# Kernel tuning notes

Hardware: AMD Instinct MI355X
Metric: run time of the kernel (lower is better)

Reference implementation:

```python
import jax, jax.numpy as jnp
import numpy as np

DIM = 256; CTX_DIM = 256; K = 7; SK = 5; NH = 4  # num_heads*2
HD = DIM // NH; SCALE = HD ** -0.5
H = 64; W = 64; HC = 56; WC = 56
LN_EPS = 1e-6; BN_EPS = 1e-5


def make_bias_idx(k, h, w):
    # Faithful port of ContMix.generate_idx + apply_rpb index construction.
    rs = 2 * k - 1
    idx_h = np.arange(k); idx_w = np.arange(k)
    idx_k = (idx_h[:, None] * rs + idx_w).reshape(-1)
    rep_h = np.ones(k, np.int64); rep_h[k // 2] = h - (k - 1)
    rep_w = np.ones(k, np.int64); rep_w[k // 2] = w - (k - 1)
    bias_hw = np.repeat(idx_h, rep_h)[:, None] * rs + np.repeat(idx_w, rep_w)  # (h, w)
    bias_idx = (bias_hw[..., None] + idx_k).reshape(-1, k * k)                 # (h*w, k^2)
    return jnp.asarray(bias_idx[::-1].copy())  # torch.flip along dim 0


def window_idx(n, k):
    # NATTEN-style clamped neighborhood window starts.
    s = np.clip(np.arange(n) - k // 2, 0, n - k)
    return jnp.asarray(s[:, None] + np.arange(k))  # (n, k)


BIDX1 = make_bias_idx(SK, H, W)
BIDX2 = make_bias_idx(K, H, W)
IDXI_S = window_idx(H, SK); IDXJ_S = window_idx(W, SK)
IDXI_L = window_idx(H, K);  IDXJ_L = window_idx(W, K)


def ln2d(x, g, b):
    # LayerNorm over channel dim per spatial location, x: (B, C, H, W)
    mu = x.mean(1, keepdims=True)
    var = ((x - mu) ** 2).mean(1, keepdims=True)
    return (x - mu) * jax.lax.rsqrt(var + LN_EPS) * g[None, :, None, None] + b[None, :, None, None]


def conv1x1(x, Wt):
    return jnp.einsum('oc,bchw->bohw', Wt, x)


def apply_rpb(attn, rpb, bias_idx, h, w):
    g = rpb.shape[0]
    r = rpb.reshape(g, -1)[:, bias_idx]  # (g, h*w, k^2)
    return attn + r.reshape(1, g, h, w, -1)


def na2d_av(attn, value, k, idx_i, idx_j):
    # attn: (B, G, H, W, k^2), value: (B, G, H, W, C)
    B, G, h, w, _ = attn.shape
    v = value[:, :, idx_i]        # (B, G, H, k, W, C)
    v = v[:, :, :, :, idx_j]      # (B, G, H, k, W, k, C)
    a = attn.reshape(B, G, h, w, k, k)
    return jnp.einsum('bghwpq,bghpwqc->bghwc', a, v)


def contmix_forward(x, ctx, Wq, gq, bq, Wk, gk, bk, Wproj, rpb1, rpb2, Wdy, bn_g, bn_b):
    B = x.shape[0]
    q = ln2d(conv1x1(x, Wq), gq, bq) * SCALE                       # (B, DIM, H, W)
    # AdaptiveAvgPool2d(7) on 56x56 -> exact 8x8 bins
    kctx = ctx.reshape(B, CTX_DIM, 7, HC // 7, 7, WC // 7).mean((3, 5))
    kf = ln2d(conv1x1(kctx, Wk), gk, bk)                            # (B, DIM, 7, 7)
    q = q.reshape(B, NH, HD, H * W)
    kf = kf.reshape(B, NH, HD, 49)
    wgt = jnp.einsum('bgcn,bgcl->bgnl', q, kf)                      # (B, 4, HW, 49)
    wgt = jnp.einsum('ml,bgnl->bgnm', Wproj, wgt)                   # (B, 4, HW, 74)
    wgt = wgt.reshape(B, NH, H, W, SK * SK + K * K)
    attn1 = wgt[:, :NH // 2, :, :, :SK * SK]                        # group1, 25
    attn2 = wgt[:, NH // 2:, :, :, SK * SK:]                        # group2, 49
    attn1 = jax.nn.softmax(apply_rpb(attn1, rpb1, BIDX1, H, W), -1)
    attn2 = jax.nn.softmax(apply_rpb(attn2, rpb2, BIDX2, H, W), -1)
    # 'b (m g c) h w -> m b g h w c', m=2, g=2
    v = x.reshape(B, 2, NH // 2, HD, H, W).transpose(1, 0, 2, 4, 5, 3)
    x1 = na2d_av(attn1, v[0], SK, IDXI_S, IDXJ_S)                   # (B, 2, H, W, HD)
    x2 = na2d_av(attn2, v[1], K, IDXI_L, IDXJ_L)
    out = jnp.concatenate([x1, x2], axis=1)                         # (B, 4, H, W, HD)
    out = out.transpose(0, 1, 4, 2, 3).reshape(B, DIM, H, W)
    out = conv1x1(out, Wdy)
    # BatchNorm2d in eval mode: running_mean=0, running_var=1
    out = out * (bn_g * jax.lax.rsqrt(jnp.float32(1.0) + BN_EPS))[None, :, None, None] + bn_b[None, :, None, None]
    return out


def setup_inputs() -> dict:
    key = jax.random.key(0)
    ks = jax.random.split(key, 10)
    d = {}
    d['x'] = jax.random.normal(ks[0], (4, DIM, H, W), jnp.float32)
    d['ctx'] = jax.random.normal(ks[1], (4, CTX_DIM, HC, WC), jnp.float32)
    d['Wq'] = jax.random.normal(ks[2], (DIM, DIM), jnp.float32) * 0.02
    d['gq'] = jnp.ones((DIM,), jnp.float32)
    d['bq'] = jnp.zeros((DIM,), jnp.float32)
    d['Wk'] = jax.random.normal(ks[3], (DIM, CTX_DIM), jnp.float32) * 0.02
    d['gk'] = jnp.ones((DIM,), jnp.float32)
    d['bk'] = jnp.zeros((DIM,), jnp.float32)
    d['Wproj'] = jax.random.normal(ks[4], (SK * SK + K * K, 49), jnp.float32) * 0.1
    d['rpb1'] = jax.random.normal(ks[5], (NH // 2, 2 * SK - 1, 2 * SK - 1), jnp.float32) * 0.02
    d['rpb2'] = jax.random.normal(ks[6], (NH // 2, 2 * K - 1, 2 * K - 1), jnp.float32) * 0.02
    d['Wdy'] = jax.random.normal(ks[7], (DIM, DIM), jnp.float32) * 0.02
    d['bn_g'] = jnp.ones((DIM,), jnp.float32)
    d['bn_b'] = jnp.zeros((DIM,), jnp.float32)
    return d


def reference(x, ctx, Wq, gq, bq, Wk, gk, bk, Wproj, rpb1, rpb2, Wdy, bn_g, bn_b):
    return contmix_forward(x, ctx, Wq, gq, bq, Wk, gk, bk, Wproj, rpb1, rpb2, Wdy, bn_g, bn_b)
```

## Files before the change

### kernel.cpp

```cpp
#include <hip/hip_runtime.h>

#define DEV __device__ __forceinline__

typedef __bf16 bf16x8 __attribute__((ext_vector_type(8)));
typedef __bf16 bf16x4 __attribute__((ext_vector_type(4)));
typedef float floatx4 __attribute__((ext_vector_type(4)));

__global__ __launch_bounds__(256)
void prep_kernel(const float* __restrict__ Wq, const float* __restrict__ Wdy,
                 const float* __restrict__ ctx, const float* __restrict__ x,
                 __bf16* __restrict__ wqb, __bf16* __restrict__ wdyb,
                 float* __restrict__ kctx, __bf16* __restrict__ xt,
                 float* __restrict__ stats) {
  __shared__ float tile[64][65];
  int bid = blockIdx.x, t = threadIdx.x;
  if (bid < 256) {
    int i = bid * 256 + t;
    wqb[i]  = (__bf16)Wq[i];
    wdyb[i] = (__bf16)Wdy[i];
  } else if (bid < 512) {
    int bc = (bid - 256) * 4 + (t >> 6);
    const float* src = ctx + (size_t)bc * (56 * 56);
    int w = t & 63;
#pragma unroll
    for (int pi = 0; pi < 7; ++pi) {
      float s = 0.f;
      if (w < 56) {
#pragma unroll
        for (int di = 0; di < 8; ++di) s += src[(pi * 8 + di) * 56 + w];
      }
      s += __shfl_down(s, 4);
      s += __shfl_down(s, 2);
      s += __shfl_down(s, 1);
      if (w < 56 && (w & 7) == 0)
        kctx[(size_t)bc * 49 + pi * 7 + (w >> 3)] = s * (1.f / 64.f);
    }
  } else if (bid < 1536) {
    int idx = bid - 512;
    int b = idx >> 8, c0 = ((idx >> 6) & 3) * 64, n0 = (idx & 63) * 64;
    int lane = t & 63, rg = t >> 6;
    const float* src = x + ((size_t)b * 256 + c0) * 4096 + n0;
    for (int i = rg; i < 64; i += 4) tile[i][lane] = src[(size_t)i * 4096 + lane];
    __syncthreads();
    __bf16* dst = xt + ((size_t)b * 4096 + n0) * 256 + c0;
    for (int i = rg; i < 64; i += 4) dst[(size_t)i * 256 + lane] = (__bf16)tile[lane][i];
  } else {
    int base = (bid - 1536) * 1024 + t * 4;
    *(float4*)&stats[base] = make_float4(0.f, 0.f, 0.f, 0.f);
  }
}

__global__ __launch_bounds__(256)
void kf_ln_kernel(const float* __restrict__ kctx, const float* __restrict__ Wk,
                  const float* __restrict__ gk, const float* __restrict__ bk,
                  float* __restrict__ kf) {
  int b = blockIdx.x / 49, l = blockIdx.x % 49;
  __shared__ float xs[256];
  __shared__ float r1[4], r2[4];
  int o = threadIdx.x;
  xs[o] = kctx[((size_t)b * 256 + o) * 49 + l];
  __syncthreads();
  const float* wrow = Wk + (size_t)o * 256;
  float acc = 0.f;
#pragma unroll 8
  for (int c = 0; c < 256; c += 4) {
    float4 wv = *(const float4*)(wrow + c);
    acc += wv.x * xs[c] + wv.y * xs[c + 1] + wv.z * xs[c + 2] + wv.w * xs[c + 3];
  }
  float s1 = acc, s2 = acc * acc;
#pragma unroll
  for (int off = 32; off > 0; off >>= 1) {
    s1 += __shfl_down(s1, off);
    s2 += __shfl_down(s2, off);
  }
  int wv_ = o >> 6, ln = o & 63;
  if (ln == 0) { r1[wv_] = s1; r2[wv_] = s2; }
  __syncthreads();
  float mu  = (r1[0] + r1[1] + r1[2] + r1[3]) * (1.f / 256.f);
  float var = (r2[0] + r2[1] + r2[2] + r2[3]) * (1.f / 256.f) - mu * mu;
  float rstd = rsqrtf(var + 1e-6f);
  kf[((size_t)b * 256 + o) * 49 + l] = (acc - mu) * rstd * gk[o] + bk[o];
}

__global__ __launch_bounds__(256)
void kfp_kernel(const float* __restrict__ kf, const float* __restrict__ Wproj,
                __bf16* __restrict__ kfpT) {
  int bg = blockIdx.x; int b = bg >> 2, g = bg & 3;
  int m0 = blockIdx.y * 16;
  __shared__ float kfs[64][50];
  __shared__ float wps[16][50];
  int t = threadIdx.x;
  for (int i = t; i < 64 * 49; i += 256) {
    int d = i / 49, l = i % 49;
    kfs[d][l] = kf[((size_t)b * 256 + g * 64 + d) * 49 + l];
  }
  for (int i = t; i < 16 * 49; i += 256) {
    int m = i / 49, l = i % 49;
    wps[m][l] = (m0 + m < 74) ? Wproj[(m0 + m) * 49 + l] : 0.f;
  }
  __syncthreads();
  for (int i = t; i < 64 * 16; i += 256) {
    int d = i >> 4, m = i & 15;
    float s = 0.f;
    if (m0 + m < 74) {
#pragma unroll 7
      for (int l = 0; l < 49; ++l) s += kfs[d][l] * wps[m][l];
    }
    kfpT[(size_t)bg * 5120 + (m0 + m) * 64 + d] = (__bf16)s;
  }
}

template <int MODE>
__global__ __launch_bounds__(256, 2)
void conv_mfma_kernel(const __bf16* __restrict__ Wb, const __bf16* __restrict__ Xin,
                      void* __restrict__ Yout, float* __restrict__ stats,
                      const float* __restrict__ bn_g, const float* __restrict__ bn_b) {
  int b  = blockIdx.z;
  int n0 = blockIdx.x * 128;
  int o0 = blockIdx.y * 128;
  __shared__ __bf16 As[128 * 32];
  __shared__ __bf16 Bs[128 * 32];
  int t = threadIdx.x;
  int lane = t & 63, wv = t >> 6;
  int mq = (wv & 1) * 64, nq = (wv >> 1) * 64;
  int col = lane & 15, quad = lane >> 4;
  floatx4 acc[4][4];
#pragma unroll
  for (int i = 0; i < 4; ++i)
#pragma unroll
    for (int j = 0; j < 4; ++j) acc[i][j] = {0.f, 0.f, 0.f, 0.f};
  int sm = t >> 1, sk = (t & 1) << 4;
  for (int c0 = 0; c0 < 256; c0 += 32) {
    const __bf16* wsrc = Wb + (size_t)(o0 + sm) * 256 + c0 + sk;
    *(bf16x8*)&As[sm * 32 + sk]     = *(const bf16x8*)wsrc;
    *(bf16x8*)&As[sm * 32 + sk + 8] = *(const bf16x8*)(wsrc + 8);
    const __bf16* xsrc;
    if (MODE == 0) {
      xsrc = Xin + ((size_t)b * 4096 + n0 + sm) * 256 + c0 + sk;
    } else {
      int c = c0 + sk, g = c >> 6, c64 = c & 63;
      xsrc = Xin + (((size_t)(b * 4 + g)) * 4096 + n0 + sm) * 64 + c64;
    }
    *(bf16x8*)&Bs[sm * 32 + sk]     = *(const bf16x8*)xsrc;
    *(bf16x8*)&Bs[sm * 32 + sk + 8] = *(const bf16x8*)(xsrc + 8);
    __syncthreads();
    bf16x8 fa[4], fb[4];
#pragma unroll
    for (int i = 0; i < 4; ++i)
      fa[i] = *(const bf16x8*)&As[(mq + i * 16 + col) * 32 + quad * 8];
#pragma unroll
    for (int j = 0; j < 4; ++j)
      fb[j] = *(const bf16x8*)&Bs[(nq + j * 16 + col) * 32 + quad * 8];
#pragma unroll
    for (int i = 0; i < 4; ++i)
#pragma unroll
      for (int j = 0; j < 4; ++j)
        acc[i][j] = __builtin_amdgcn_mfma_f32_16x16x32_bf16(fa[i], fb[j], acc[i][j], 0, 0, 0);
    __syncthreads();
  }
  if (MODE == 0) {
    __bf16* QT = (__bf16*)Yout + (size_t)b * 4096 * 256;
    float s_j[4] = {0.f, 0.f, 0.f, 0.f}, q_j[4] = {0.f, 0.f, 0.f, 0.f};
#pragma unroll
    for (int i = 0; i < 4; ++i) {
#pragma unroll
      for (int j = 0; j < 4; ++j) {
        int o = o0 + mq + i * 16 + quad * 4;
        int n = n0 + nq + j * 16 + col;
        __bf16 pk[4];
#pragma unroll
        for (int r = 0; r < 4; ++r) {
          float v = acc[i][j][r];
          s_j[j] += v; q_j[j] += v * v;
          pk[r] = (__bf16)v;
        }
        *(bf16x4*)&QT[(size_t)n * 256 + o] = *(bf16x4*)pk;
      }
    }
#pragma unroll
    for (int j = 0; j < 4; ++j) {
      float s = s_j[j], qq = q_j[j];
      s  += __shfl_down(s, 32);  s  += __shfl_down(s, 16);
      qq += __shfl_down(qq, 32); qq += __shfl_down(qq, 16);
      if (quad == 0) {
        int n = n0 + nq + j * 16 + col;
        atomicAdd(&stats[(size_t)b * 4096 + n], s);
        atomicAdd(&stats[16384 + (size_t)b * 4096 + n], qq);
      }
    }
  } else {
    float* Yf = (float*)Yout + (size_t)b * 256 * 4096;
#pragma unroll
    for (int i = 0; i < 4; ++i) {
#pragma unroll
      for (int r = 0; r < 4; ++r) {
        int o = o0 + mq + i * 16 + quad * 4 + r;
        float scale = bn_g[o] * 0.9999950000374997f;
        float shift = bn_b[o];
        float* yrow = Yf + (size_t)o * 4096 + n0 + nq + col;
#pragma unroll
        for (int j = 0; j < 4; ++j) yrow[j * 16] = acc[i][j][r] * scale + shift;
      }
    }
  }
}

DEV int rep_idx(int p, int kc, int t1, int sub) {
  return p < kc ? p : (p < t1 ? kc : p - sub);
}

template <int KK>
DEV void softmax_write(const float* wms, const float* rpb_s, __bf16* __restrict__ attnL,
                       int bg, int n_glob, int t) {
  constexpr int CNT = KK * KK;
  constexpr int RS  = 2 * KK - 1;
  constexpr int KC  = KK / 2;
  constexpr int T1  = KC + (64 - KK + 1);
  constexpr int SUB = 64 - KK;
  constexpr int MLO = (KK == 5) ? 0 : 25;
  constexpr int PW  = (KK == 5) ? 32 : 56;
  int h = n_glob >> 6, w = n_glob & 63;
  int rh = rep_idx(63 - h, KC, T1, SUB);
  int rw = rep_idx(63 - w, KC, T1, SUB);
  float vals[CNT];
  float mx = -1e30f;
#pragma unroll
  for (int m = 0; m < CNT; ++m) {
    int ki = m / KK, kj = m % KK;
    float v = wms[t * 81 + MLO + m] + rpb_s[(rh + ki) * RS + rw + kj];
    vals[m] = v; mx = fmaxf(mx, v);
  }
  float ssum = 0.f;
#pragma unroll
  for (int m = 0; m < CNT; ++m) { float e = __expf(vals[m] - mx); vals[m] = e; ssum += e; }
  float inv = 1.f / ssum;
  __bf16 hv[PW];
#pragma unroll
  for (int m = 0; m < PW; ++m) hv[m] = (__bf16)(m < CNT ? vals[m] * inv : 0.f);
  __bf16* ap = attnL + ((size_t)bg * 4096 + n_glob) * 56;
#pragma unroll
  for (int i = 0; i < PW / 8; ++i) *(bf16x8*)(ap + i * 8) = *(bf16x8*)&hv[i * 8];
}

__global__ __launch_bounds__(256)
void attn_kernel(const __bf16* __restrict__ qT, const float* __restrict__ stats,
                 const float* __restrict__ gq, const float* __restrict__ bq,
                 const __bf16* __restrict__ kfpT, const float* __restrict__ rpb1,
                 const float* __restrict__ rpb2, __bf16* __restrict__ attnL) {
  __shared__ uint32_t smem4[10368];
  __shared__ float rpb_s[169];
  __bf16* A_s = (__bf16*)smem4;
  __bf16* B_s = (__bf16*)smem4 + 9216;
  float* wms  = (float*)smem4;
  int bg = blockIdx.x; int b = bg >> 2, g = bg & 3;
  int n0 = blockIdx.y * 128;
  int t = threadIdx.x;
  for (int idx = t; idx < 1024; idx += 256) {
    int n = idx >> 3, d8 = idx & 7;
    int ng = n0 + n;
    float s  = stats[(size_t)b * 4096 + ng];
    float ss = stats[16384 + (size_t)b * 4096 + ng];
    float mu = s * (1.f / 256.f);
    float rs = rsqrtf(ss * (1.f / 256.f) - mu * mu + 1e-6f);
    bf16x8 raw = *(const bf16x8*)&qT[((size_t)b * 4096 + ng) * 256 + g * 64 + d8 * 8];
    __bf16 tmp[8];
#pragma unroll
    for (int e = 0; e < 8; ++e) {
      int d = g * 64 + d8 * 8 + e;
      tmp[e] = (__bf16)((((float)raw[e]) - mu) * rs * (gq[d] * 0.125f) + bq[d] * 0.125f);
    }
    *(bf16x8*)&A_s[n * 72 + d8 * 8] = *(bf16x8*)tmp;
  }
  for (int idx = t; idx < 640; idx += 256)
    *(bf16x8*)&B_s[(idx >> 3) * 72 + (idx & 7) * 8] = *(const bf16x8*)&kfpT[(size_t)bg * 5120 + idx * 8];
  if (g < 2) { for (int i = t; i <  81; i += 256) rpb_s[i] = rpb1[g * 81 + i]; }
  else       { for (int i = t; i < 169; i += 256) rpb_s[i] = rpb2[(g - 2) * 169 + i]; }
  __syncthreads();
  int lane = t & 63, wv = t >> 6;
  int col = lane & 15, quad = lane >> 4;
  floatx4 acc[2][5];
#pragma unroll
  for (int mi = 0; mi < 2; ++mi)
#pragma unroll
    for (int nt = 0; nt < 5; ++nt) acc[mi][nt] = {0.f, 0.f, 0.f, 0.f};
  bf16x8 fa[2][2], fb[2][5];
#pragma unroll
  for (int ks = 0; ks < 2; ++ks) {
#pragma unroll
    for (int mi = 0; mi < 2; ++mi)
      fa[ks][mi] = *(const bf16x8*)&A_s[((wv * 2 + mi) * 16 + col) * 72 + ks * 32 + quad * 8];
#pragma unroll
    for (int nt = 0; nt < 5; ++nt)
      fb[ks][nt] = *(const bf16x8*)&B_s[(nt * 16 + col) * 72 + ks * 32 + quad * 8];
  }
#pragma unroll
  for (int ks = 0; ks < 2; ++ks)
#pragma unroll
    for (int mi = 0; mi < 2; ++mi)
#pragma unroll
      for (int nt = 0; nt < 5; ++nt)
        acc[mi][nt] = __builtin_amdgcn_mfma_f32_16x16x32_bf16(fa[ks][mi], fb[ks][nt], acc[mi][nt], 0, 0, 0);
  __syncthreads();
#pragma unroll
  for (int mi = 0; mi < 2; ++mi)
#pragma unroll
    for (int nt = 0; nt < 5; ++nt)
#pragma unroll
      for (int r = 0; r < 4; ++r)
        wms[((wv * 2 + mi) * 16 + quad * 4 + r) * 81 + nt * 16 + col] = acc[mi][nt][r];
  __syncthreads();
  if (t < 128) {
    int n_glob = n0 + t;
    if (g < 2) softmax_write<5>(wms, rpb_s, attnL, bg, n_glob, t);
    else       softmax_write<7>(wms, rpb_s, attnL, bg, n_glob, t);
  }
}

template <int KK>
DEV void na2d_body(const __bf16* __restrict__ attnL, const __bf16* __restrict__ XT,
                   __bf16* __restrict__ midT, __bf16* xs, int bg, int h0, int chalf, int t) {
  constexpr int CNT = KK * KK, KC = KK / 2, SMAX = 64 - KK;
  constexpr int ROWS = KK + 3;
  constexpr int PW = (KK == 5) ? 32 : 56;
  int b = bg >> 2, g = bg & 3;
  int si0 = min(max(h0 - KC, 0), SMAX);
  {
    int sn = t >> 2, sc = t & 3;
    const __bf16* src = XT + ((size_t)b * 4096 + sn) * 256 + g * 64 + chalf * 32 + sc * 8;
#pragma unroll
    for (int r = 0; r < ROWS; ++r) {
      int gr = min(si0 + r, 63);
      *(bf16x8*)&xs[(r * 64 + sn) * 40 + sc * 8] = *(const bf16x8*)(src + (size_t)gr * 64 * 256);
    }
  }
  __syncthreads();
  int w = t >> 2, cg = t & 3;
  int sj = min(max(w - KC, 0), SMAX);
#pragma unroll
  for (int h4 = 0; h4 < 4; ++h4) {
    int h = h0 + h4;
    int base = min(max(h - KC, 0), SMAX) - si0;
    bf16x8 avh[PW / 8];
    const __bf16* ap = attnL + ((size_t)bg * 4096 + h * 64 + w) * 56;
#pragma unroll
    for (int i = 0; i < PW / 8; ++i) avh[i] = *(const bf16x8*)(ap + i * 8);
    float av[CNT];
#pragma unroll
    for (int m = 0; m < CNT; ++m) av[m] = (float)avh[m / 8][m % 8];
    float acc[8] = {};
#pragma unroll
    for (int p = 0; p < KK; ++p) {
      const __bf16* xr = &xs[((base + p) * 64 + sj) * 40 + cg * 8];
#pragma unroll
      for (int q = 0; q < KK; ++q) {
        bf16x8 v = *(const bf16x8*)(xr + q * 40);
        float a = av[p * KK + q];
#pragma unroll
        for (int e = 0; e < 8; ++e) acc[e] += a * (float)v[e];
      }
    }
    __bf16 hv[8];
#pragma unroll
    for (int e = 0; e < 8; ++e) hv[e] = (__bf16)acc[e];
    *(bf16x8*)&midT[((size_t)bg * 4096 + h * 64 + w) * 64 + chalf * 32 + cg * 8] = *(bf16x8*)hv;
  }
}

__global__ __launch_bounds__(256)
void na2d_kernel(const __bf16* __restrict__ attnL, const __bf16* __restrict__ XT,
                 __bf16* __restrict__ midT) {
  __shared__ __bf16 xs[10 * 64 * 40];
  int bg = blockIdx.x, h0 = blockIdx.y * 4, chalf = blockIdx.z, t = threadIdx.x;
  if ((bg & 3) < 2) na2d_body<5>(attnL, XT, midT, xs, bg, h0, chalf, t);
  else              na2d_body<7>(attnL, XT, midT, xs, bg, h0, chalf, t);
}

extern "C" void kernel_launch(void* const* d_in, const int* in_sizes, int n_in,
                              void* d_out, int out_size, void* d_ws, size_t ws_size,
                              hipStream_t stream) {
  const float* x     = (const float*)d_in[0];
  const float* ctx   = (const float*)d_in[1];
  const float* Wq    = (const float*)d_in[2];
  const float* gq    = (const float*)d_in[3];
  const float* bq    = (const float*)d_in[4];
  const float* Wk    = (const float*)d_in[5];
  const float* gk    = (const float*)d_in[6];
  const float* bk    = (const float*)d_in[7];
  const float* Wproj = (const float*)d_in[8];
  const float* rpb1  = (const float*)d_in[9];
  const float* rpb2  = (const float*)d_in[10];
  const float* Wdy   = (const float*)d_in[11];
  const float* bn_g  = (const float*)d_in[12];
  const float* bn_b  = (const float*)d_in[13];
  float* out = (float*)d_out;

  float* ws     = (float*)d_ws;
  float* kctx   = ws;
  float* kf     = kctx + 50176;
  float* stats  = kf + 50176;
  __bf16* attnL = (__bf16*)(stats + 32768);
  __bf16* wqb   = attnL + 3670016;
  __bf16* wdyb  = wqb + 65536;
  __bf16* kfpT  = wdyb + 65536;
  __bf16* XT    = kfpT + 81920;
  __bf16* qT    = XT + 4194304;
  __bf16* midT  = qT + 4194304;

  prep_kernel<<<dim3(1568), dim3(256), 0, stream>>>(Wq, Wdy, ctx, x, wqb, wdyb, kctx, XT, stats);
  kf_ln_kernel<<<dim3(196), dim3(256), 0, stream>>>(kctx, Wk, gk, bk, kf);
  kfp_kernel<<<dim3(16, 5), dim3(256), 0, stream>>>(kf, Wproj, kfpT);
  conv_mfma_kernel<0><<<dim3(32, 2, 4), dim3(256), 0, stream>>>(wqb, XT, qT, stats, nullptr, nullptr);
  attn_kernel<<<dim3(16, 32), dim3(256), 0, stream>>>(qT, stats, gq, bq, kfpT, rpb1, rpb2, attnL);
  na2d_kernel<<<dim3(16, 16, 2), dim3(256), 0, stream>>>(attnL, XT, midT);
  conv_mfma_kernel<1><<<dim3(32, 2, 4), dim3(256), 0, stream>>>(wdyb, midT, out, nullptr, bn_g, bn_b);
}
```

Measured before the change: 164.7 us.

## Fuse channel LayerNorm into Q conv with full-channel tiles, drop atomic stats

The Q projection kernel now computes all 256 output channels for a 32-pixel tile in one block. This lets it reduce LayerNorm mean and variance in shared memory and write an already-normalized, scaled q. The global atomic stats buffer, its zeroing in the prep kernel, and the per-element normalization in the attention kernel's load are removed. In exchange, each block reloads the full 256x256 weight matrix from L2 for only 32 pixels, so the smaller N tile adds weight traffic and reduces MFMA reuse.

```diff
diff --git a/kernel.cpp b/kernel.cpp
--- a/kernel.cpp
+++ b/kernel.cpp
@@ -10,8 +10,7 @@
 void prep_kernel(const float* __restrict__ Wq, const float* __restrict__ Wdy,
                  const float* __restrict__ ctx, const float* __restrict__ x,
                  __bf16* __restrict__ wqb, __bf16* __restrict__ wdyb,
-                 float* __restrict__ kctx, __bf16* __restrict__ xt,
-                 float* __restrict__ stats) {
+                 float* __restrict__ kctx, __bf16* __restrict__ xt) {
   __shared__ float tile[64][65];
   int bid = blockIdx.x, t = threadIdx.x;
   if (bid < 256) {
@@ -35,7 +34,7 @@
       if (w < 56 && (w & 7) == 0)
         kctx[(size_t)bc * 49 + pi * 7 + (w >> 3)] = s * (1.f / 64.f);
     }
-  } else if (bid < 1536) {
+  } else {
     int idx = bid - 512;
     int b = idx >> 8, c0 = ((idx >> 6) & 3) * 64, n0 = (idx & 63) * 64;
     int lane = t & 63, rg = t >> 6;
@@ -44,9 +43,6 @@
     __syncthreads();
     __bf16* dst = xt + ((size_t)b * 4096 + n0) * 256 + c0;
     for (int i = rg; i < 64; i += 4) dst[(size_t)i * 256 + lane] = (__bf16)tile[lane][i];
-  } else {
-    int base = (bid - 1536) * 1024 + t * 4;
-    *(float4*)&stats[base] = make_float4(0.f, 0.f, 0.f, 0.f);
   }
 }
 
@@ -110,11 +106,100 @@
   }
 }
 
-template <int MODE>
 __global__ __launch_bounds__(256, 2)
-void conv_mfma_kernel(const __bf16* __restrict__ Wb, const __bf16* __restrict__ Xin,
-                      void* __restrict__ Yout, float* __restrict__ stats,
-                      const float* __restrict__ bn_g, const float* __restrict__ bn_b) {
+void conv_q_kernel(const __bf16* __restrict__ Wb, const __bf16* __restrict__ XT,
+                   const float* __restrict__ gq, const float* __restrict__ bq,
+                   __bf16* __restrict__ qT) {
+  __shared__ __bf16 As[256 * 32];
+  __shared__ __bf16 Bs[32 * 32];
+  __shared__ float gs[256], bs[256];
+  __shared__ float red[4][2][16][2];
+  __shared__ float mu_s[32], rs_s[32];
+  int b = blockIdx.y;
+  int n0 = blockIdx.x * 32;
+  int t = threadIdx.x, lane = t & 63, wv = t >> 6;
+  int col = lane & 15, quad = lane >> 4;
+  gs[t] = gq[t] * 0.125f;
+  bs[t] = bq[t] * 0.125f;
+  floatx4 acc[4][2];
+#pragma unroll
+  for (int mi = 0; mi < 4; ++mi)
+#pragma unroll
+    for (int nj = 0; nj < 2; ++nj) acc[mi][nj] = {0.f, 0.f, 0.f, 0.f};
+  for (int c0 = 0; c0 < 256; c0 += 32) {
+    const __bf16* wsrc = Wb + (size_t)t * 256 + c0;
+    *(bf16x8*)&As[t * 32 + 0]  = *(const bf16x8*)(wsrc);
+    *(bf16x8*)&As[t * 32 + 8]  = *(const bf16x8*)(wsrc + 8);
+    *(bf16x8*)&As[t * 32 + 16] = *(const bf16x8*)(wsrc + 16);
+    *(bf16x8*)&As[t * 32 + 24] = *(const bf16x8*)(wsrc + 24);
+    if (t < 128) {
+      int n = t >> 2, k8 = (t & 3) * 8;
+      *(bf16x8*)&Bs[n * 32 + k8] =
+          *(const bf16x8*)(XT + ((size_t)b * 4096 + n0 + n) * 256 + c0 + k8);
+    }
+    __syncthreads();
+    bf16x8 fa[4], fb[2];
+#pragma unroll
+    for (int mi = 0; mi < 4; ++mi)
+      fa[mi] = *(const bf16x8*)&As[(wv * 64 + mi * 16 + col) * 32 + quad * 8];
+#pragma unroll
+    for (int nj = 0; nj < 2; ++nj)
+      fb[nj] = *(const bf16x8*)&Bs[(nj * 16 + col) * 32 + quad * 8];
+#pragma unroll
+    for (int mi = 0; mi < 4; ++mi)
+#pragma unroll
+      for (int nj = 0; nj < 2; ++nj)
+        acc[mi][nj] = __builtin_amdgcn_mfma_f32_16x16x32_bf16(fa[mi], fb[nj], acc[mi][nj], 0, 0, 0);
+    __syncthreads();
+  }
+  float s[2] = {0.f, 0.f}, sq[2] = {0.f, 0.f};
+#pragma unroll
+  for (int mi = 0; mi < 4; ++mi)
+#pragma unroll
+    for (int nj = 0; nj < 2; ++nj)
+#pragma unroll
+      for (int r = 0; r < 4; ++r) {
+        float v = acc[mi][nj][r];
+        s[nj] += v; sq[nj] += v * v;
+      }
+#pragma unroll
+  for (int nj = 0; nj < 2; ++nj) {
+    float a = s[nj], q = sq[nj];
+    a += __shfl_down(a, 32); a += __shfl_down(a, 16);
+    q += __shfl_down(q, 32); q += __shfl_down(q, 16);
+    if (quad == 0) { red[wv][nj][col][0] = a; red[wv][nj][col][1] = q; }
+  }
+  __syncthreads();
+  if (t < 32) {
+    int nj = t >> 4, cc = t & 15;
+    float S = red[0][nj][cc][0] + red[1][nj][cc][0] + red[2][nj][cc][0] + red[3][nj][cc][0];
+    float Q = red[0][nj][cc][1] + red[1][nj][cc][1] + red[2][nj][cc][1] + red[3][nj][cc][1];
+    float mu = S * (1.f / 256.f);
+    float var = Q * (1.f / 256.f) - mu * mu;
+    mu_s[t] = mu; rs_s[t] = rsqrtf(var + 1e-6f);
+  }
+  __syncthreads();
+  __bf16* QT = qT + (size_t)b * 4096 * 256;
+#pragma unroll
+  for (int mi = 0; mi < 4; ++mi) {
+#pragma unroll
+    for (int nj = 0; nj < 2; ++nj) {
+      int o = wv * 64 + mi * 16 + quad * 4;
+      int nl = nj * 16 + col;
+      float mu = mu_s[nl], rs = rs_s[nl];
+      __bf16 pk[4];
+#pragma unroll
+      for (int r = 0; r < 4; ++r)
+        pk[r] = (__bf16)((acc[mi][nj][r] - mu) * rs * gs[o + r] + bs[o + r]);
+      *(bf16x4*)&QT[(size_t)(n0 + nl) * 256 + o] = *(bf16x4*)pk;
+    }
+  }
+}
+
+__global__ __launch_bounds__(256, 2)
+void conv_out_kernel(const __bf16* __restrict__ Wb, const __bf16* __restrict__ Xin,
+                     float* __restrict__ Yout,
+                     const float* __restrict__ bn_g, const float* __restrict__ bn_b) {
   int b  = blockIdx.z;
   int n0 = blockIdx.x * 128;
   int o0 = blockIdx.y * 128;
@@ -134,13 +219,8 @@
     const __bf16* wsrc = Wb + (size_t)(o0 + sm) * 256 + c0 + sk;
     *(bf16x8*)&As[sm * 32 + sk]     = *(const bf16x8*)wsrc;
     *(bf16x8*)&As[sm * 32 + sk + 8] = *(const bf16x8*)(wsrc + 8);
-    const __bf16* xsrc;
-    if (MODE == 0) {
-      xsrc = Xin + ((size_t)b * 4096 + n0 + sm) * 256 + c0 + sk;
-    } else {
-      int c = c0 + sk, g = c >> 6, c64 = c & 63;
-      xsrc = Xin + (((size_t)(b * 4 + g)) * 4096 + n0 + sm) * 64 + c64;
-    }
+    int c = c0 + sk, g = c >> 6, c64 = c & 63;
+    const __bf16* xsrc = Xin + (((size_t)(b * 4 + g)) * 4096 + n0 + sm) * 64 + c64;
     *(bf16x8*)&Bs[sm * 32 + sk]     = *(const bf16x8*)xsrc;
     *(bf16x8*)&Bs[sm * 32 + sk + 8] = *(const bf16x8*)(xsrc + 8);
     __syncthreads();
@@ -158,49 +238,17 @@
         acc[i][j] = __builtin_amdgcn_mfma_f32_16x16x32_bf16(fa[i], fb[j], acc[i][j], 0, 0, 0);
     __syncthreads();
   }
-  if (MODE == 0) {
-    __bf16* QT = (__bf16*)Yout + (size_t)b * 4096 * 256;
-    float s_j[4] = {0.f, 0.f, 0.f, 0.f}, q_j[4] = {0.f, 0.f, 0.f, 0.f};
-#pragma unroll
-    for (int i = 0; i < 4; ++i) {
-#pragma unroll
-      for (int j = 0; j < 4; ++j) {
-        int o = o0 + mq + i * 16 + quad * 4;
-        int n = n0 + nq + j * 16 + col;
-        __bf16 pk[4];
-#pragma unroll
-        for (int r = 0; r < 4; ++r) {
-          float v = acc[i][j][r];
-          s_j[j] += v; q_j[j] += v * v;
-          pk[r] = (__bf16)v;
-        }
-        *(bf16x4*)&QT[(size_t)n * 256 + o] = *(bf16x4*)pk;
-      }
-    }
-#pragma unroll
-    for (int j = 0; j < 4; ++j) {
-      float s = s_j[j], qq = q_j[j];
-      s  += __shfl_down(s, 32);  s  += __shfl_down(s, 16);
-      qq += __shfl_down(qq, 32); qq += __shfl_down(qq, 16);
-      if (quad == 0) {
-        int n = n0 + nq + j * 16 + col;
-        atomicAdd(&stats[(size_t)b * 4096 + n], s);
-        atomicAdd(&stats[16384 + (size_t)b * 4096 + n], qq);
-      }
-    }
-  } else {
-    float* Yf = (float*)Yout + (size_t)b * 256 * 4096;
-#pragma unroll
-    for (int i = 0; i < 4; ++i) {
-#pragma unroll
-      for (int r = 0; r < 4; ++r) {
-        int o = o0 + mq + i * 16 + quad * 4 + r;
-        float scale = bn_g[o] * 0.9999950000374997f;
-        float shift = bn_b[o];
-        float* yrow = Yf + (size_t)o * 4096 + n0 + nq + col;
-#pragma unroll
-        for (int j = 0; j < 4; ++j) yrow[j * 16] = acc[i][j][r] * scale + shift;
-      }
+  float* Yf = Yout + (size_t)b * 256 * 4096;
+#pragma unroll
+  for (int i = 0; i < 4; ++i) {
+#pragma unroll
+    for (int r = 0; r < 4; ++r) {
+      int o = o0 + mq + i * 16 + quad * 4 + r;
+      float scale = bn_g[o] * 0.9999950000374997f;
+      float shift = bn_b[o];
+      float* yrow = Yf + (size_t)o * 4096 + n0 + nq + col;
+#pragma unroll
+      for (int j = 0; j < 4; ++j) yrow[j * 16] = acc[i][j][r] * scale + shift;
     }
   }
 }
@@ -243,10 +291,9 @@
 }
 
 __global__ __launch_bounds__(256)
-void attn_kernel(const __bf16* __restrict__ qT, const float* __restrict__ stats,
-                 const float* __restrict__ gq, const float* __restrict__ bq,
-                 const __bf16* __restrict__ kfpT, const float* __restrict__ rpb1,
-                 const float* __restrict__ rpb2, __bf16* __restrict__ attnL) {
+void attn_kernel(const __bf16* __restrict__ qT, const __bf16* __restrict__ kfpT,
+                 const float* __restrict__ rpb1, const float* __restrict__ rpb2,
+                 __bf16* __restrict__ attnL) {
   __shared__ uint32_t smem4[10368];
   __shared__ float rpb_s[169];
   __bf16* A_s = (__bf16*)smem4;
@@ -257,19 +304,8 @@
   int t = threadIdx.x;
   for (int idx = t; idx < 1024; idx += 256) {
     int n = idx >> 3, d8 = idx & 7;
-    int ng = n0 + n;
-    float s  = stats[(size_t)b * 4096 + ng];
-    float ss = stats[16384 + (size_t)b * 4096 + ng];
-    float mu = s * (1.f / 256.f);
-    float rs = rsqrtf(ss * (1.f / 256.f) - mu * mu + 1e-6f);
-    bf16x8 raw = *(const bf16x8*)&qT[((size_t)b * 4096 + ng) * 256 + g * 64 + d8 * 8];
-    __bf16 tmp[8];
-#pragma unroll
-    for (int e = 0; e < 8; ++e) {
-      int d = g * 64 + d8 * 8 + e;
-      tmp[e] = (__bf16)((((float)raw[e]) - mu) * rs * (gq[d] * 0.125f) + bq[d] * 0.125f);
-    }
-    *(bf16x8*)&A_s[n * 72 + d8 * 8] = *(bf16x8*)tmp;
+    *(bf16x8*)&A_s[n * 72 + d8 * 8] =
+        *(const bf16x8*)&qT[((size_t)b * 4096 + n0 + n) * 256 + g * 64 + d8 * 8];
   }
   for (int idx = t; idx < 640; idx += 256)
     *(bf16x8*)&B_s[(idx >> 3) * 72 + (idx & 7) * 8] = *(const bf16x8*)&kfpT[(size_t)bg * 5120 + idx * 8];
@@ -397,8 +433,7 @@
   float* ws     = (float*)d_ws;
   float* kctx   = ws;
   float* kf     = kctx + 50176;
-  float* stats  = kf + 50176;
-  __bf16* attnL = (__bf16*)(stats + 32768);
+  __bf16* attnL = (__bf16*)(kf + 50176);
   __bf16* wqb   = attnL + 3670016;
   __bf16* wdyb  = wqb + 65536;
   __bf16* kfpT  = wdyb + 65536;
@@ -406,11 +441,11 @@
   __bf16* qT    = XT + 4194304;
   __bf16* midT  = qT + 4194304;
 
-  prep_kernel<<<dim3(1568), dim3(256), 0, stream>>>(Wq, Wdy, ctx, x, wqb, wdyb, kctx, XT, stats);
+  prep_kernel<<<dim3(1536), dim3(256), 0, stream>>>(Wq, Wdy, ctx, x, wqb, wdyb, kctx, XT);
   kf_ln_kernel<<<dim3(196), dim3(256), 0, stream>>>(kctx, Wk, gk, bk, kf);
   kfp_kernel<<<dim3(16, 5), dim3(256), 0, stream>>>(kf, Wproj, kfpT);
-  conv_mfma_kernel<0><<<dim3(32, 2, 4), dim3(256), 0, stream>>>(wqb, XT, qT, stats, nullptr, nullptr);
-  attn_kernel<<<dim3(16, 32), dim3(256), 0, stream>>>(qT, stats, gq, bq, kfpT, rpb1, rpb2, attnL);
+  conv_q_kernel<<<dim3(128, 4), dim3(256), 0, stream>>>(wqb, XT, gq, bq, qT);
+  attn_kernel<<<dim3(16, 32), dim3(256), 0, stream>>>(qT, kfpT, rpb1, rpb2, attnL);
   na2d_kernel<<<dim3(16, 16, 2), dim3(256), 0, stream>>>(attnL, XT, midT);
-  conv_mfma_kernel<1><<<dim3(32, 2, 4), dim3(256), 0, stream>>>(wdyb, midT, out, nullptr, bn_g, bn_b);
-}
+  conv_out_kernel<<<dim3(32, 2, 4), dim3(256), 0, stream>>>(wdyb, midT, out, bn_g, bn_b);
+}
```

Result: slower. 169.7 us (+3.1%).
